# Kernel optimization log

Measured on AMD Instinct MI355X. Metric: run time of the kernel, lower is better.

## Reference

```python
import jax, jax.numpy as jnp
import numpy as np

B, S, HID = 2, 2048, 2048
H, KH, D = 16, 4, 128  # heads, kv heads, head_dim
N_REP = H // KH
SCALE = D ** -0.5


def rotate_half(x):
    x1, x2 = x[..., : D // 2], x[..., D // 2:]
    return jnp.concatenate((-x2, x1), axis=-1)


def setup_inputs() -> dict:
    key = jax.random.key(0)
    ks = jax.random.split(key, 6)
    hidden_states = jax.random.normal(ks[0], (B, S, HID), jnp.float32)
    # standard RoPE cos/sin tables, shape [B, S, D]
    inv_freq = 1.0 / (10000.0 ** (np.arange(0, D, 2, dtype=np.float32) / D))
    pos = np.arange(S, dtype=np.float32)
    freqs = np.outer(pos, inv_freq)            # [S, D/2]
    emb = np.concatenate([freqs, freqs], -1)   # [S, D]
    cos = jnp.broadcast_to(jnp.cos(emb), (B, S, D)).astype(jnp.float32)
    sin = jnp.broadcast_to(jnp.sin(emb), (B, S, D)).astype(jnp.float32)
    # additive causal mask [1, 1, S, S]
    neg = jnp.finfo(jnp.float32).min
    causal = jnp.triu(jnp.full((S, S), neg, jnp.float32), k=1)
    attention_mask = causal[None, None]
    std = 0.02
    wq = jax.random.normal(ks[1], (HID, H * D), jnp.float32) * std
    wk = jax.random.normal(ks[2], (HID, KH * D), jnp.float32) * std
    wv = jax.random.normal(ks[3], (HID, KH * D), jnp.float32) * std
    wo = jax.random.normal(ks[4], (H * D, HID), jnp.float32) * std
    return {"hidden_states": hidden_states, "cos": cos, "sin": sin,
            "attention_mask": attention_mask, "wq": wq, "wk": wk, "wv": wv, "wo": wo}


def reference(hidden_states, cos, sin, attention_mask, wq, wk, wv, wo):
    b, s, _ = hidden_states.shape
    q = (hidden_states @ wq).reshape(b, s, H, D).transpose(0, 2, 1, 3)   # [b,H,s,d]
    k = (hidden_states @ wk).reshape(b, s, KH, D).transpose(0, 2, 1, 3)  # [b,KH,s,d]
    v = (hidden_states @ wv).reshape(b, s, KH, D).transpose(0, 2, 1, 3)
    c = cos[:, None, :, :]  # [b,1,s,d] broadcast over heads
    sn = sin[:, None, :, :]
    q = q * c + rotate_half(q) * sn
    k = k * c + rotate_half(k) * sn
    # GQA: repeat KV heads
    k = jnp.repeat(k, N_REP, axis=1)  # [b,H,s,d]
    v = jnp.repeat(v, N_REP, axis=1)
    scores = jnp.einsum('bhqd,bhkd->bhqk', q, k) * SCALE + attention_mask
    probs = jax.nn.softmax(scores, axis=-1)
    attn = jnp.einsum('bhqk,bhkd->bhqd', probs, v)
    attn = attn.transpose(0, 2, 1, 3).reshape(b, s, H * D)
    return attn @ wo
```

## Files before the change

kernel.cpp:

```cpp
#include <hip/hip_runtime.h>
#include <stdint.h>

#define Bc   2
#define Sc   2048
#define HIDc 2048
#define Hc   16
#define KHc  4
#define Dc   128
#define HDc  2048
#define KHDc 512
#define QKVS 3072
#define SCALE2c 0.12751744657f
#define M0c 6.0f
#define N_ITEMS2 768

typedef _Float16 f16;
typedef _Float16 f16x2 __attribute__((ext_vector_type(2)));
typedef _Float16 f16x4 __attribute__((ext_vector_type(4)));
typedef _Float16 f16x8 __attribute__((ext_vector_type(8)));
typedef float    f32x4 __attribute__((ext_vector_type(4)));

__device__ __forceinline__ void gl_lds16(const void* g, void* l) {
  __builtin_amdgcn_global_load_lds(
      (const __attribute__((address_space(1))) unsigned int*)g,
      (__attribute__((address_space(3))) unsigned int*)l, 16, 0, 0);
}

__global__ __launch_bounds__(256) void conv_hs(const float* __restrict__ in,
                                               f16* __restrict__ out,
                                               int* __restrict__ ctr) {
  if (blockIdx.x == 0 && threadIdx.x == 0) *ctr = 0;
  int i = (blockIdx.x * 256 + threadIdx.x) * 4;
  float4 v = *(const float4*)&in[i];
  f16x4 o; o[0] = (f16)v.x; o[1] = (f16)v.y; o[2] = (f16)v.z; o[3] = (f16)v.w;
  *(f16x4*)&out[i] = o;
}

__global__ __launch_bounds__(256) void trw_all(const float* __restrict__ wq,
                                               const float* __restrict__ wk,
                                               const float* __restrict__ wv,
                                               const float* __restrict__ wo,
                                               f16* __restrict__ wqkvT,
                                               f16* __restrict__ woT) {
  const int z = blockIdx.z;
  const float* in; f16* out; int C, rowOff;
  if (z == 0)      { in = wq; out = wqkvT; C = 2048; rowOff = 0; }
  else if (z == 1) { in = wk; out = wqkvT; C = 512;  rowOff = 2048; }
  else if (z == 2) { in = wv; out = wqkvT; C = 512;  rowOff = 2560; }
  else             { in = wo; out = woT;   C = 2048; rowOff = 0; }
  if (blockIdx.x * 64 >= C) return;
  __shared__ float Ld[64 * 65];
  const int tid = threadIdx.x;
  const int r0 = blockIdx.y * 64, c0 = blockIdx.x * 64;
#pragma unroll
  for (int p = 0; p < 4; ++p) {
    int idx = p * 256 + tid;
    int r = idx >> 4, c4 = (idx & 15) * 4;
    float4 v = *(const float4*)&in[(size_t)(r0 + r) * C + c0 + c4];
    Ld[r * 65 + c4 + 0] = v.x; Ld[r * 65 + c4 + 1] = v.y;
    Ld[r * 65 + c4 + 2] = v.z; Ld[r * 65 + c4 + 3] = v.w;
  }
  __syncthreads();
#pragma unroll
  for (int p = 0; p < 4; ++p) {
    int idx = p * 256 + tid;
    int oc = idx >> 4, m4 = (idx & 15) * 4;
    f16x4 o;
#pragma unroll
    for (int i = 0; i < 4; ++i) o[i] = (f16)Ld[(m4 + i) * 65 + oc];
    *(f16x4*)&out[(size_t)(rowOff + c0 + oc) * 2048 + r0 + m4] = o;
  }
}

__global__ __launch_bounds__(256) void rope_all(f16* __restrict__ x,
                                                const float* __restrict__ cb,
                                                const float* __restrict__ sb) {
  int bid = blockIdx.x;
  int colbase, log2h, idx;
  if (bid < 16384) { colbase = 0;    log2h = 4; idx = bid * 256 + threadIdx.x; }
  else             { colbase = 2048; log2h = 2; idx = (bid - 16384) * 256 + threadIdx.x; }
  int d   = idx & 63;
  int h   = (idx >> 6) & ((1 << log2h) - 1);
  int row = idx >> (6 + log2h);
  f16* p = x + (size_t)row * QKVS + colbase + h * 128;
  float x1 = (float)p[d], x2 = (float)p[64 + d];
  float c = cb[(size_t)row * 128 + d], s = sb[(size_t)row * 128 + d];
  p[d]      = (f16)(x1 * c - x2 * s);
  p[64 + d] = (f16)(x2 * c + x1 * s);
}

__global__ __launch_bounds__(256) void v_tr(const f16* __restrict__ QKV,
                                            f16* __restrict__ Vt) {
  __shared__ f16 Ld[64 * 78];
  const int tid = threadIdx.x;
  const int s0 = blockIdx.x * 64, d0 = blockIdx.y * 64;
  const int b = blockIdx.z >> 2, kh = blockIdx.z & 3;
#pragma unroll
  for (int p = 0; p < 2; ++p) {
    int idx = p * 256 + tid;
    int sl = idx >> 3, dc8 = (idx & 7) * 8;
    f16x8 v = *(const f16x8*)&QKV[(size_t)(b * Sc + s0 + sl) * QKVS + 2560 + kh * 128 + d0 + dc8];
#pragma unroll
    for (int i = 0; i < 4; ++i) {
      f16x2 w; w[0] = v[2 * i]; w[1] = v[2 * i + 1];
      *(f16x2*)&Ld[sl * 78 + dc8 + 2 * i] = w;
    }
  }
  __syncthreads();
  {
    int dr = (tid >> 3) * 2, sc8 = (tid & 7) * 8;
    f16x8 r0v, r1v;
#pragma unroll
    for (int j = 0; j < 8; ++j) {
      f16x2 w = *(const f16x2*)&Ld[(sc8 + j) * 78 + dr];
      r0v[j] = w[0]; r1v[j] = w[1];
    }
    size_t obase = ((size_t)(b * KHc + kh) * 128 + d0 + dr) * Sc + s0 + sc8;
    *(f16x8*)&Vt[obase]      = r0v;
    *(f16x8*)&Vt[obase + Sc] = r1v;
  }
}

template<int NREP, int CF16>
__global__ __launch_bounds__(512, 2) void gemm8p(const f16* __restrict__ A,
                                                 const f16* __restrict__ Bt,
                                                 void* __restrict__ Cout,
                                                 int K, int cstride) {
  __shared__ f16 Al[2][16384];
  __shared__ f16 Bl[2][NREP * 4096];
  const int tid  = threadIdx.x;
  const int lane = tid & 63, wave = tid >> 6;
  const int quad = lane >> 4, l16 = lane & 15;
  const int wm = wave >> 2, wn = wave & 3;
  const int m0 = blockIdx.y * 256, n0 = blockIdx.x * (NREP * 64);
  f32x4 acc[8][NREP] = {};

  auto stage = [&](int buf, int k0) {
#pragma unroll
    for (int p = 0; p < 4; ++p) {
      const int g  = wave * 2 + (p >> 1);
      const int kq = (p & 1) * 4 + quad;
      gl_lds16(&A[(size_t)(m0 + g * 16 + l16) * K + k0 + kq * 8],
               &Al[buf][(wave * 4 + p) * 512]);
    }
#pragma unroll
    for (int p = 0; p < NREP; ++p) {
      const int gb = wave * NREP + p;
      const int gi = gb >> 1, kh2 = gb & 1;
      gl_lds16(&Bt[(size_t)(n0 + gi * 16 + l16) * K + k0 + kh2 * 32 + quad * 8],
               &Bl[buf][gb * 512]);
    }
  };

  stage(0, 0);
  const int NT = K >> 6;
  for (int t = 0; t < NT; ++t) {
    const int cur = t & 1;
    __syncthreads();
    if (t + 1 < NT) stage(cur ^ 1, (t + 1) * 64);

    f16x8 bf[NREP][2];
#pragma unroll
    for (int j = 0; j < NREP; ++j)
#pragma unroll
      for (int ks = 0; ks < 2; ++ks)
        bf[j][ks] = *(const f16x8*)&Bl[cur][(((wn * NREP + j) * 8 + ks * 4 + quad) * 16 + l16) * 8];
#pragma unroll
    for (int mh = 0; mh < 2; ++mh) {
      f16x8 af[4][2];
#pragma unroll
      for (int i = 0; i < 4; ++i)
#pragma unroll
        for (int ks = 0; ks < 2; ++ks)
          af[i][ks] = *(const f16x8*)&Al[cur][(((wm * 8 + mh * 4 + i) * 8 + ks * 4 + quad) * 16 + l16) * 8];
      __builtin_amdgcn_s_setprio(1);
#pragma unroll
      for (int ks = 0; ks < 2; ++ks)
#pragma unroll
        for (int i = 0; i < 4; ++i)
#pragma unroll
          for (int j = 0; j < NREP; ++j)
            acc[mh * 4 + i][j] = __builtin_amdgcn_mfma_f32_16x16x32_f16(
                af[i][ks], bf[j][ks], acc[mh * 4 + i][j], 0, 0, 0);
      __builtin_amdgcn_s_setprio(0);
    }
  }

  const int rbase = m0 + wm * 128;
  const int cbase = n0 + wn * NREP * 16;
#pragma unroll
  for (int mi = 0; mi < 8; ++mi)
#pragma unroll
    for (int j = 0; j < NREP; ++j)
#pragma unroll
      for (int r = 0; r < 4; ++r) {
        size_t idx = (size_t)(rbase + mi * 16 + quad * 4 + r) * cstride + cbase + j * 16 + l16;
        if (CF16) ((f16*)Cout)[idx]   = (f16)acc[mi][j][r];
        else      ((float*)Cout)[idx] = acc[mi][j][r];
      }
}

__global__ __launch_bounds__(512, 4) void attn_v8(const f16* __restrict__ QKV,
                                                  const f16* __restrict__ Vt,
                                                  f16* __restrict__ Ob,
                                                  f16* __restrict__ Opart,
                                                  float2* __restrict__ ML,
                                                  int* __restrict__ ctr) {
  __shared__ f16 Kl[2][8192];
  __shared__ f16 Vl[2][8192];
  __shared__ f16 Ps[8 * 512];
  __shared__ int item_s;
  const int tid  = threadIdx.x;
  const int lane = tid & 63, wave = tid >> 6;
  const int quad = lane >> 4, l16 = lane & 15;
  const int qsel = wave >> 2, wv = wave & 3;

  f16x8 ones_f;
#pragma unroll
  for (int i = 0; i < 8; ++i) ones_f[i] = (l16 == 0) ? (f16)1.0f : (f16)0.0f;

  for (;;) {
    if (tid == 0) item_s = atomicAdd(ctr, 1);
    __syncthreads();
    const int item = item_s;
    if (item >= N_ITEMS2) break;

    int p, bh, k0t, k1t, hf = -1;
    if (item < 640) {
      int base = 0, c = 16;
#pragma unroll 1
      for (; c >= 9; --c) {
        int sz = (c & 1) ? 64 : 96;
        if (item < base + sz) break;
        base += sz;
      }
      int off = item - base;
      if (off < 64) {
        p = c - 1; hf = off >> 5; bh = off & 31;
        int hn = p + 1;
        k0t = hf ? hn : 0; k1t = hf ? 2 * p + 2 : hn;
      } else {
        p = (c >> 1) - 1; bh = off - 64; k0t = 0; k1t = 2 * p + 2;
      }
    } else {
      int off = item - 640;
      p = 3 - (off >> 5); bh = off & 31; k0t = 0; k1t = 2 * p + 2;
    }
    const int b = bh >> 4, h = bh & 15, kh = h >> 2;
    const int qt = 2 * p + qsel;
    const int qbase = qt * 64 + wv * 16;

    f16x8 qf[4];
    {
      const f16* qp = QKV + (size_t)(b * Sc + qbase + l16) * QKVS + h * 128 + quad * 8;
#pragma unroll
      for (int c = 0; c < 4; ++c) qf[c] = *(const f16x8*)(qp + c * 32);
    }
    f32x4 ls = {};
    f32x4 o[8] = {};

    auto stageKV = [&](int kt, int buf) {
#pragma unroll
      for (int p2 = 0; p2 < 2; ++p2) {
        const int g = wave * 2 + p2;
        gl_lds16(&QKV[(size_t)(b * Sc + kt * 64 + (g >> 2) * 16 + l16) * QKVS + 2048 + kh * 128 + (g & 3) * 32 + quad * 8],
                 &Kl[buf][g * 512]);
      }
#pragma unroll
      for (int p2 = 0; p2 < 2; ++p2) {
        const int g = wave * 2 + p2;
        gl_lds16(&Vt[(size_t)((b * KHc + kh) * 128 + (g >> 1) * 16 + l16) * Sc + kt * 64 + (g & 1) * 32 + quad * 8],
                 &Vl[buf][g * 512]);
      }
    };

    stageKV(k0t, 0);
    stageKV(k0t + 1, 1);

    for (int kt = k0t; kt < k1t; ++kt) {
      const int cur = (kt - k0t) & 1;
      if (kt + 1 < k1t) { asm volatile("s_waitcnt vmcnt(4)" ::: "memory"); }
      else              { asm volatile("s_waitcnt vmcnt(0)" ::: "memory"); }
      __builtin_amdgcn_sched_barrier(0);
      __builtin_amdgcn_s_barrier();
      __builtin_amdgcn_sched_barrier(0);

      if (kt <= qt) {
        __builtin_amdgcn_s_setprio(1);
        f32x4 s4[4] = {};
#pragma unroll
        for (int kc = 0; kc < 2; ++kc)
#pragma unroll
          for (int c = 0; c < 4; ++c) {
            f16x8 ka = *(const f16x8*)&Kl[cur][(((kc * 2 + 0) * 4 + c) * 4 + quad) * 128 + l16 * 8];
            f16x8 kb = *(const f16x8*)&Kl[cur][(((kc * 2 + 1) * 4 + c) * 4 + quad) * 128 + l16 * 8];
            s4[kc * 2 + 0] = __builtin_amdgcn_mfma_f32_16x16x32_f16(qf[c], ka, s4[kc * 2 + 0], 0, 0, 0);
            s4[kc * 2 + 1] = __builtin_amdgcn_mfma_f32_16x16x32_f16(qf[c], kb, s4[kc * 2 + 1], 0, 0, 0);
          }
        __builtin_amdgcn_s_setprio(0);

        const bool diag = (kt == qt);
        const int cb = kt * 64 + l16;
        const int wb  = wave * 512 + (l16 & 7);
        const int rhi = l16 >> 3;
        float e2[4], e3[4];
#pragma unroll
        for (int r = 0; r < 4; ++r) {
          float v0 = fmaf(s4[0][r], SCALE2c, -M0c);
          float v1 = fmaf(s4[1][r], SCALE2c, -M0c);
          float v2 = fmaf(s4[2][r], SCALE2c, -M0c);
          float v3 = fmaf(s4[3][r], SCALE2c, -M0c);
          if (diag) {
            const int qrow = qbase + quad * 4 + r;
            if (cb      > qrow) v0 = -1e30f;
            if (cb + 16 > qrow) v1 = -1e30f;
            if (cb + 32 > qrow) v2 = -1e30f;
            if (cb + 48 > qrow) v3 = -1e30f;
          }
          float p0 = exp2f(v0), p1 = exp2f(v1);
          e2[r] = exp2f(v2); e3[r] = exp2f(v3);
          const int rowoff = (quad * 4 + r) * 8;
          Ps[wb + (rhi + 0) * 128 + rowoff] = (f16)p0;
          Ps[wb + (rhi + 2) * 128 + rowoff] = (f16)p1;
        }

        {
          f16x8 pf = *(const f16x8*)&Ps[wave * 512 + quad * 128 + l16 * 8];
          __builtin_amdgcn_s_setprio(1);
          ls = __builtin_amdgcn_mfma_f32_16x16x32_f16(pf, ones_f, ls, 0, 0, 0);
#pragma unroll
          for (int dt = 0; dt < 8; ++dt) {
            f16x8 vf = *(const f16x8*)&Vl[cur][((dt * 2 + 0) * 4 + quad) * 128 + l16 * 8];
            o[dt] = __builtin_amdgcn_mfma_f32_16x16x32_f16(pf, vf, o[dt], 0, 0, 0);
          }
          __builtin_amdgcn_s_setprio(0);
        }
#pragma unroll
        for (int r = 0; r < 4; ++r) {
          const int rowoff = (quad * 4 + r) * 8;
          Ps[wb + (rhi + 0) * 128 + rowoff] = (f16)e2[r];
          Ps[wb + (rhi + 2) * 128 + rowoff] = (f16)e3[r];
        }
        {
          f16x8 pf = *(const f16x8*)&Ps[wave * 512 + quad * 128 + l16 * 8];
          __builtin_amdgcn_s_setprio(1);
          ls = __builtin_amdgcn_mfma_f32_16x16x32_f16(pf, ones_f, ls, 0, 0, 0);
#pragma unroll
          for (int dt = 0; dt < 8; ++dt) {
            f16x8 vf = *(const f16x8*)&Vl[cur][((dt * 2 + 1) * 4 + quad) * 128 + l16 * 8];
            o[dt] = __builtin_amdgcn_mfma_f32_16x16x32_f16(pf, vf, o[dt], 0, 0, 0);
          }
          __builtin_amdgcn_s_setprio(0);
        }
      }

      __builtin_amdgcn_sched_barrier(0);
      __builtin_amdgcn_s_barrier();
      __builtin_amdgcn_sched_barrier(0);
      if (kt + 2 < k1t) stageKV(kt + 2, cur);
    }

    float inv[4], lrow[4];
#pragma unroll
    for (int r = 0; r < 4; ++r) {
      lrow[r] = __shfl(ls[r], lane & 48);
      inv[r] = 1.0f / lrow[r];
    }
    const int rl = wv * 16 + quad * 4;
    if (hf < 0) {
#pragma unroll
      for (int dt = 0; dt < 8; ++dt)
#pragma unroll
        for (int r = 0; r < 4; ++r)
          Ob[(size_t)(b * Sc + qbase + quad * 4 + r) * HDc + h * 128 + dt * 16 + l16] =
              (f16)(o[dt][r] * inv[r]);
    } else {
      const int tile = (qt - 16) * 32 + bh;
      f16* op = Opart + ((size_t)tile * 2 + hf) * (64 * 128);
#pragma unroll
      for (int dt = 0; dt < 8; ++dt)
#pragma unroll
        for (int r = 0; r < 4; ++r)
          op[(rl + r) * 128 + dt * 16 + l16] = (f16)(o[dt][r] * inv[r]);
      if (l16 == 0) {
#pragma unroll
        for (int r = 0; r < 4; ++r) {
          float2 ml; ml.x = M0c; ml.y = lrow[r];
          ML[((size_t)tile * 2 + hf) * 64 + rl + r] = ml;
        }
      }
    }
  }
}

__global__ __launch_bounds__(256) void attn_merge(const f16* __restrict__ Opart,
                                                  const float2* __restrict__ ML,
                                                  f16* __restrict__ Ob) {
  const int tile = blockIdx.x;
  const int qt = 16 + (tile >> 5), bh = tile & 31;
  const int b = bh >> 4, h = bh & 15;
  const int tid = threadIdx.x;
  const int row = tid >> 2, c0 = (tid & 3) * 32;
  float2 ml1 = ML[(size_t)tile * 2 * 64 + row];
  float2 ml2 = ML[((size_t)tile * 2 + 1) * 64 + row];
  float m = fmaxf(ml1.x, ml2.x);
  float w1 = ml1.y * exp2f(ml1.x - m);
  float w2 = ml2.y * exp2f(ml2.x - m);
  float rinv = 1.0f / (w1 + w2);
  float a1 = w1 * rinv, a2 = w2 * rinv;
  const f16* o1 = Opart + (size_t)tile * 2 * (64 * 128) + row * 128 + c0;
  const f16* o2 = o1 + 64 * 128;
  f16* out = Ob + (size_t)(b * Sc + qt * 64 + row) * HDc + h * 128 + c0;
#pragma unroll
  for (int j = 0; j < 4; ++j) {
    f16x8 x1 = *(const f16x8*)(o1 + j * 8);
    f16x8 x2 = *(const f16x8*)(o2 + j * 8);
    f16x8 y;
#pragma unroll
    for (int i = 0; i < 8; ++i) y[i] = (f16)(a1 * (float)x1[i] + a2 * (float)x2[i]);
    *(f16x8*)(out + j * 8) = y;
  }
}

extern "C" void kernel_launch(void* const* d_in, const int* in_sizes, int n_in,
                              void* d_out, int out_size, void* d_ws, size_t ws_size,
                              hipStream_t stream) {
  (void)in_sizes; (void)n_in; (void)out_size; (void)ws_size;
  const float* hs   = (const float*)d_in[0];
  const float* cosb = (const float*)d_in[1];
  const float* sinb = (const float*)d_in[2];
  const float* wq = (const float*)d_in[4];
  const float* wk = (const float*)d_in[5];
  const float* wv = (const float*)d_in[6];
  const float* wo = (const float*)d_in[7];
  float* out = (float*)d_out;

  char* ws = (char*)d_ws;
  int*  ctr = (int*)ws;
  size_t off = 256;
  auto alloc = [&](size_t bytes) { char* p = ws + off; off += (bytes + 255) & ~(size_t)255; return p; };
  f16*  hsF   = (f16*)alloc((size_t)Bc * Sc * HIDc * 2);
  f16*  woT   = (f16*)alloc((size_t)HIDc * HDc * 2);
  f16*  QKVf  = (f16*)alloc((size_t)Bc * Sc * QKVS * 2);
  f16*  Vt_g  = (f16*)alloc((size_t)Bc * KHc * Dc * Sc * 2);
  f16*  wqkvT = (f16*)alloc((size_t)QKVS * HIDc * 2);
  f16*  Opart = wqkvT;
  {
    size_t opart_bytes = (size_t)512 * 2 * 64 * 128 * 2;
    size_t wqkvT_bytes = (size_t)QKVS * HIDc * 2;
    if (opart_bytes > wqkvT_bytes) off += opart_bytes - wqkvT_bytes;
  }
  float2* ML = (float2*)alloc((size_t)512 * 2 * 64 * sizeof(float2));
  f16*  attnF = hsF;

  conv_hs<<<8192, 256, 0, stream>>>(hs, hsF, ctr);
  trw_all<<<dim3(32, 32, 4), 256, 0, stream>>>(wq, wk, wv, wo, wqkvT, woT);

  gemm8p<3, 1><<<dim3(16, 16), 512, 0, stream>>>(hsF, wqkvT, QKVf, 2048, QKVS);

  rope_all<<<20480, 256, 0, stream>>>(QKVf, cosb, sinb);
  v_tr<<<dim3(32, 2, 8), 256, 0, stream>>>(QKVf, Vt_g);

  attn_v8<<<512, 512, 0, stream>>>(QKVf, Vt_g, attnF, Opart, ML, ctr);
  attn_merge<<<512, 256, 0, stream>>>(Opart, ML, attnF);

  gemm8p<2, 0><<<dim3(16, 16), 512, 0, stream>>>(attnF, woT, out, 2048, 2048);
}
```

Measured before the change: 397.2 us.

## Halve GEMM M-tile to 128 rows and vectorize RoPE to 8 elements per thread

```diff
diff --git a/kernel.cpp b/kernel.cpp
--- a/kernel.cpp
+++ b/kernel.cpp
@@ -72,21 +72,32 @@
   }
 }
 
-__global__ __launch_bounds__(256) void rope_all(f16* __restrict__ x,
-                                                const float* __restrict__ cb,
-                                                const float* __restrict__ sb) {
+__global__ __launch_bounds__(256) void rope8(f16* __restrict__ x,
+                                             const float* __restrict__ cb,
+                                             const float* __restrict__ sb) {
   int bid = blockIdx.x;
-  int colbase, log2h, idx;
-  if (bid < 16384) { colbase = 0;    log2h = 4; idx = bid * 256 + threadIdx.x; }
-  else             { colbase = 2048; log2h = 2; idx = (bid - 16384) * 256 + threadIdx.x; }
-  int d   = idx & 63;
-  int h   = (idx >> 6) & ((1 << log2h) - 1);
-  int row = idx >> (6 + log2h);
-  f16* p = x + (size_t)row * QKVS + colbase + h * 128;
-  float x1 = (float)p[d], x2 = (float)p[64 + d];
-  float c = cb[(size_t)row * 128 + d], s = sb[(size_t)row * 128 + d];
-  p[d]      = (f16)(x1 * c - x2 * s);
-  p[64 + d] = (f16)(x2 * c + x1 * s);
+  int colbase, idx, h, row;
+  if (bid < 2048) { idx = bid * 256 + threadIdx.x; colbase = 0;    h = (idx >> 3) & 15; row = idx >> 7; }
+  else            { idx = (bid - 2048) * 256 + threadIdx.x; colbase = 2048; h = (idx >> 3) & 3;  row = idx >> 5; }
+  const int d0 = (idx & 7) * 8;
+  f16* p = x + (size_t)row * QKVS + colbase + h * 128 + d0;
+  f16x8 x1 = *(const f16x8*)p;
+  f16x8 x2 = *(const f16x8*)(p + 64);
+  const float* cp = cb + (size_t)row * 128 + d0;
+  const float* sp = sb + (size_t)row * 128 + d0;
+  float4 c0 = *(const float4*)cp, c1 = *(const float4*)(cp + 4);
+  float4 s0 = *(const float4*)sp, s1 = *(const float4*)(sp + 4);
+  float cc[8] = {c0.x, c0.y, c0.z, c0.w, c1.x, c1.y, c1.z, c1.w};
+  float ss[8] = {s0.x, s0.y, s0.z, s0.w, s1.x, s1.y, s1.z, s1.w};
+  f16x8 y1, y2;
+#pragma unroll
+  for (int i = 0; i < 8; ++i) {
+    float a = (float)x1[i], b = (float)x2[i];
+    y1[i] = (f16)(a * cc[i] - b * ss[i]);
+    y2[i] = (f16)(b * cc[i] + a * ss[i]);
+  }
+  *(f16x8*)p = y1;
+  *(f16x8*)(p + 64) = y2;
 }
 
 __global__ __launch_bounds__(256) void v_tr(const f16* __restrict__ QKV,
@@ -122,26 +133,24 @@
 }
 
 template<int NREP, int CF16>
-__global__ __launch_bounds__(512, 2) void gemm8p(const f16* __restrict__ A,
-                                                 const f16* __restrict__ Bt,
-                                                 void* __restrict__ Cout,
-                                                 int K, int cstride) {
-  __shared__ f16 Al[2][16384];
+__global__ __launch_bounds__(512, 4) void gemm128(const f16* __restrict__ A,
+                                                  const f16* __restrict__ Bt,
+                                                  void* __restrict__ Cout,
+                                                  int K, int cstride) {
+  __shared__ f16 Al[2][8192];
   __shared__ f16 Bl[2][NREP * 4096];
   const int tid  = threadIdx.x;
   const int lane = tid & 63, wave = tid >> 6;
   const int quad = lane >> 4, l16 = lane & 15;
   const int wm = wave >> 2, wn = wave & 3;
-  const int m0 = blockIdx.y * 256, n0 = blockIdx.x * (NREP * 64);
-  f32x4 acc[8][NREP] = {};
+  const int m0 = blockIdx.y * 128, n0 = blockIdx.x * (NREP * 64);
+  f32x4 acc[4][NREP] = {};
 
   auto stage = [&](int buf, int k0) {
 #pragma unroll
-    for (int p = 0; p < 4; ++p) {
-      const int g  = wave * 2 + (p >> 1);
-      const int kq = (p & 1) * 4 + quad;
-      gl_lds16(&A[(size_t)(m0 + g * 16 + l16) * K + k0 + kq * 8],
-               &Al[buf][(wave * 4 + p) * 512]);
+    for (int p = 0; p < 2; ++p) {
+      gl_lds16(&A[(size_t)(m0 + wave * 16 + l16) * K + k0 + p * 32 + quad * 8],
+               &Al[buf][(wave * 2 + p) * 512]);
     }
 #pragma unroll
     for (int p = 0; p < NREP; ++p) {
@@ -164,32 +173,29 @@
     for (int j = 0; j < NREP; ++j)
 #pragma unroll
       for (int ks = 0; ks < 2; ++ks)
-        bf[j][ks] = *(const f16x8*)&Bl[cur][(((wn * NREP + j) * 8 + ks * 4 + quad) * 16 + l16) * 8];
-#pragma unroll
-    for (int mh = 0; mh < 2; ++mh) {
-      f16x8 af[4][2];
+        bf[j][ks] = *(const f16x8*)&Bl[cur][((wn * NREP + j) * 2 + ks) * 512 + quad * 128 + l16 * 8];
+    f16x8 af[4][2];
+#pragma unroll
+    for (int i = 0; i < 4; ++i)
+#pragma unroll
+      for (int ks = 0; ks < 2; ++ks)
+        af[i][ks] = *(const f16x8*)&Al[cur][((wm * 4 + i) * 2 + ks) * 512 + quad * 128 + l16 * 8];
+    __builtin_amdgcn_s_setprio(1);
+#pragma unroll
+    for (int ks = 0; ks < 2; ++ks)
 #pragma unroll
       for (int i = 0; i < 4; ++i)
 #pragma unroll
-        for (int ks = 0; ks < 2; ++ks)
-          af[i][ks] = *(const f16x8*)&Al[cur][(((wm * 8 + mh * 4 + i) * 8 + ks * 4 + quad) * 16 + l16) * 8];
-      __builtin_amdgcn_s_setprio(1);
-#pragma unroll
-      for (int ks = 0; ks < 2; ++ks)
-#pragma unroll
-        for (int i = 0; i < 4; ++i)
-#pragma unroll
-          for (int j = 0; j < NREP; ++j)
-            acc[mh * 4 + i][j] = __builtin_amdgcn_mfma_f32_16x16x32_f16(
-                af[i][ks], bf[j][ks], acc[mh * 4 + i][j], 0, 0, 0);
-      __builtin_amdgcn_s_setprio(0);
-    }
-  }
-
-  const int rbase = m0 + wm * 128;
+        for (int j = 0; j < NREP; ++j)
+          acc[i][j] = __builtin_amdgcn_mfma_f32_16x16x32_f16(
+              af[i][ks], bf[j][ks], acc[i][j], 0, 0, 0);
+    __builtin_amdgcn_s_setprio(0);
+  }
+
+  const int rbase = m0 + wm * 64;
   const int cbase = n0 + wn * NREP * 16;
 #pragma unroll
-  for (int mi = 0; mi < 8; ++mi)
+  for (int mi = 0; mi < 4; ++mi)
 #pragma unroll
     for (int j = 0; j < NREP; ++j)
 #pragma unroll
@@ -456,13 +462,13 @@
   conv_hs<<<8192, 256, 0, stream>>>(hs, hsF, ctr);
   trw_all<<<dim3(32, 32, 4), 256, 0, stream>>>(wq, wk, wv, wo, wqkvT, woT);
 
-  gemm8p<3, 1><<<dim3(16, 16), 512, 0, stream>>>(hsF, wqkvT, QKVf, 2048, QKVS);
-
-  rope_all<<<20480, 256, 0, stream>>>(QKVf, cosb, sinb);
+  gemm128<3, 1><<<dim3(16, 32), 512, 0, stream>>>(hsF, wqkvT, QKVf, 2048, QKVS);
+
+  rope8<<<2560, 256, 0, stream>>>(QKVf, cosb, sinb);
   v_tr<<<dim3(32, 2, 8), 256, 0, stream>>>(QKVf, Vt_g);
 
   attn_v8<<<512, 512, 0, stream>>>(QKVf, Vt_g, attnF, Opart, ML, ctr);
   attn_merge<<<512, 256, 0, stream>>>(Opart, ML, attnF);
 
-  gemm8p<2, 0><<<dim3(16, 16), 512, 0, stream>>>(attnF, woT, out, 2048, 2048);
-}
+  gemm128<2, 0><<<dim3(16, 32), 512, 0, stream>>>(attnF, woT, out, 2048, 2048);
+}
```

After: 382.5 us. -3.7%, faster.
